# Performance work log

Hardware: AMD Instinct MI355X
Metric: run time of the kernel (lower is better)

Reference implementation:

```python
import jax, jax.numpy as jnp
import numpy as np

N_NODES = 50000
N_EDGES = 600000
NUM_GRAPHS = 512
IN_CH, HID, OUT_CH = 128, 128, 2


def _sage_conv(x, src, dst, Wl, Wr, b):
    # PyG SAGEConv (aggr='mean'): out = lin_l(mean_j x_j) + lin_r(x_i) + bias
    msg = x[src]  # [E, F] gather from source nodes
    agg = jax.ops.segment_sum(msg, dst, num_segments=N_NODES)
    deg = jax.ops.segment_sum(jnp.ones((src.shape[0], 1), x.dtype), dst,
                              num_segments=N_NODES)
    agg = agg / jnp.maximum(deg, 1.0)
    return agg @ Wl + x @ Wr + b


def setup_inputs() -> dict:
    key = jax.random.key(0)
    ks = jax.random.split(key, 12)
    x = jax.random.normal(ks[0], (N_NODES, IN_CH), dtype=jnp.float32)
    edge_index = jax.random.randint(ks[1], (2, N_EDGES), 0, N_NODES, dtype=jnp.int64)
    batch = jnp.sort(jax.random.randint(ks[2], (N_NODES,), 0, NUM_GRAPHS, dtype=jnp.int64))
    dims = [(IN_CH, HID), (HID, HID), (HID, HID), (HID, OUT_CH)]
    params = {}
    for i, (fi, fo) in enumerate(dims, start=1):
        s = 1.0 / np.sqrt(fi)
        params[f"W{i}l"] = jax.random.normal(ks[2 * i + 1], (fi, fo), jnp.float32) * s
        params[f"W{i}r"] = jax.random.normal(ks[2 * i + 2], (fi, fo), jnp.float32) * s
        params[f"b{i}"] = jnp.zeros((fo,), jnp.float32)
    return {"x": x, "edge_index": edge_index, "batch": batch, **params}


def reference(x, edge_index, batch,
              W1l, W1r, b1, W2l, W2r, b2, W3l, W3r, b3, W4l, W4r, b4):
    src, dst = edge_index[0], edge_index[1]
    h = jax.nn.relu(_sage_conv(x, src, dst, W1l, W1r, b1))  # dropout = identity (eval)
    h = jax.nn.relu(_sage_conv(h, src, dst, W2l, W2r, b2))
    h = jax.nn.relu(_sage_conv(h, src, dst, W3l, W3r, b3))
    h = _sage_conv(h, src, dst, W4l, W4r, b4)
    # global_mean_pool: per-graph mean over nodes
    gsum = jax.ops.segment_sum(h, batch, num_segments=NUM_GRAPHS)
    gcnt = jax.ops.segment_sum(jnp.ones((h.shape[0], 1), h.dtype), batch,
                               num_segments=NUM_GRAPHS)
    return gsum / jnp.maximum(gcnt, 1.0)  # [NUM_GRAPHS, OUT_CH]
```

## Files before the change

### kernel.cpp

```cpp
#include <hip/hip_runtime.h>

#define F 128
#define NGRAPH 512

typedef __attribute__((ext_vector_type(8))) __bf16 bf16x8;
typedef __attribute__((ext_vector_type(4))) float f32x4;
typedef __attribute__((ext_vector_type(8))) unsigned short u16x8;

__device__ __forceinline__ unsigned short f2bf(float f) {
    unsigned int u = __float_as_uint(f);
    u = (u + 0x7fffu + ((u >> 16) & 1u)) >> 16;
    return (unsigned short)u;
}
__device__ __forceinline__ float bf2f(unsigned short b) {
    return __uint_as_float(((unsigned int)b) << 16);
}


__global__ __launch_bounds__(256) void k_hist(const int* __restrict__ dst,
                                              int* __restrict__ counts, int e) {
    int i = blockIdx.x * 256 + threadIdx.x;
    if (i < e) atomicAdd(&counts[dst[i]], 1);
}

__global__ __launch_bounds__(256) void k_bsum(const int* __restrict__ counts,
                                              int* __restrict__ bsum, int n) {
    __shared__ int sm[256];
    const int t = threadIdx.x;
    int i = blockIdx.x * 256 + t;
    sm[t] = (i < n) ? counts[i] : 0;
    __syncthreads();
    for (int off = 128; off > 0; off >>= 1) {
        if (t < off) sm[t] += sm[t + off];
        __syncthreads();
    }
    if (t == 0) bsum[blockIdx.x] = sm[0];
}

__global__ __launch_bounds__(256) void k_scanb(const int* __restrict__ bsum,
                                               int* __restrict__ boff, int nb,
                                               int* __restrict__ rs, int n) {
    __shared__ int sm[256];
    const int t = threadIdx.x;
    const int npt = (nb + 255) >> 8;
    const int base = t * npt;
    int s = 0;
    for (int i = 0; i < npt; i++) { int idx = base + i; if (idx < nb) s += bsum[idx]; }
    sm[t] = s;
    __syncthreads();
    for (int off = 1; off < 256; off <<= 1) {
        int u = (t >= off) ? sm[t - off] : 0;
        __syncthreads();
        sm[t] += u;
        __syncthreads();
    }
    int run = (t == 0) ? 0 : sm[t - 1];
    for (int i = 0; i < npt; i++) {
        int idx = base + i;
        if (idx < nb) { boff[idx] = run; run += bsum[idx]; }
    }
    if (t == 255) rs[n] = sm[255];
}

__global__ __launch_bounds__(256) void k_apply(const int* __restrict__ counts,
                                               const int* __restrict__ boff,
                                               int* __restrict__ rs,
                                               int* __restrict__ cursor, int n) {
    __shared__ int sm[256];
    const int t = threadIdx.x;
    int i = blockIdx.x * 256 + t;
    int v = (i < n) ? counts[i] : 0;
    sm[t] = v;
    __syncthreads();
    for (int off = 1; off < 256; off <<= 1) {
        int u = (t >= off) ? sm[t - off] : 0;
        __syncthreads();
        sm[t] += u;
        __syncthreads();
    }
    int excl = sm[t] - v + boff[blockIdx.x];
    if (i < n) { rs[i] = excl; cursor[i] = excl; }
}

__global__ __launch_bounds__(256) void k_scatter(const int* __restrict__ src,
                                                 const int* __restrict__ dst,
                                                 int* __restrict__ cursor,
                                                 int* __restrict__ csr, int e) {
    int i = blockIdx.x * 256 + threadIdx.x;
    if (i < e) {
        int p = atomicAdd(&cursor[dst[i]], 1);
        csr[p] = src[i];
    }
}

__global__ void k_gbounds(const int* __restrict__ batch, int* __restrict__ gstart,
                          int n, int ng) {
    int g = blockIdx.x * blockDim.x + threadIdx.x;
    if (g > ng) return;
    if (g == ng) { gstart[ng] = n; return; }
    int lo = 0, hi = n;
    while (lo < hi) {
        int mid = (lo + hi) >> 1;
        if (batch[mid] < g) lo = mid + 1; else hi = mid;
    }
    gstart[g] = lo;
}


__global__ __launch_bounds__(256) void k_wprep3(
    const float* __restrict__ W1l, const float* __restrict__ W1r,
    const float* __restrict__ W2l, const float* __restrict__ W2r,
    const float* __restrict__ W3l, const float* __restrict__ W3r,
    unsigned short* __restrict__ whi, unsigned short* __restrict__ wlo) {
    int tid = blockIdx.x * 256 + threadIdx.x;
    if (tid >= 3 * 32768) return;
    int layer = tid >> 15;
    int t = tid & 32767;
    const float* Wl = (layer == 0) ? W1l : ((layer == 1) ? W2l : W3l);
    const float* Wr = (layer == 0) ? W1r : ((layer == 1) ? W2r : W3r);
    int j = t & 7;
    int fp = t >> 3;
    int l = fp & 63;
    int ks = (fp >> 6) & 7;
    int nt = fp >> 9;
    int k = ks * 32 + ((l >> 4) << 3) + j;
    int n = nt * 16 + (l & 15);
    float v = (k < F) ? Wl[k * F + n] : Wr[(k - F) * F + n];
    unsigned short hi = f2bf(v);
    unsigned short lo = f2bf(v - bf2f(hi));
    whi[tid] = hi;
    wlo[tid] = lo;
}


__global__ __launch_bounds__(256) void k_xprep(const float4* __restrict__ x4,
                                               unsigned short* __restrict__ hi,
                                               unsigned short* __restrict__ lo, int n4) {
    int i = blockIdx.x * 256 + threadIdx.x;
    if (i >= n4) return;
    float4 v = x4[i];
    ushort4 h, l;
    h.x = f2bf(v.x); l.x = f2bf(v.x - bf2f(h.x));
    h.y = f2bf(v.y); l.y = f2bf(v.y - bf2f(h.y));
    h.z = f2bf(v.z); l.z = f2bf(v.z - bf2f(h.z));
    h.w = f2bf(v.w); l.w = f2bf(v.w - bf2f(h.w));
    *(ushort4*)&hi[i * 4] = h;
    *(ushort4*)&lo[i * 4] = l;
}


__global__ __launch_bounds__(256) void k_aggm_bf(
    const unsigned short* __restrict__ hbf, const int* __restrict__ rs,
    const int* __restrict__ csr,
    unsigned short* __restrict__ agghi, unsigned short* __restrict__ agglo, int nnodes)
{
    int v = blockIdx.x * 16 + (threadIdx.x >> 4);
    if (v >= nnodes) return;
    int c = threadIdx.x & 15;
    const u16x8* h8 = (const u16x8*)hbf;
    int e0 = rs[v], e1 = rs[v + 1];

    float s0[8] = {}, s1[8] = {}, s2[8] = {}, s3[8] = {};
    int e = e0;
    for (; e + 4 <= e1; e += 4) {
        int a = csr[e], b = csr[e + 1], c2 = csr[e + 2], d = csr[e + 3];
        u16x8 va = h8[a * 16 + c];
        u16x8 vb = h8[b * 16 + c];
        u16x8 vc = h8[c2 * 16 + c];
        u16x8 vd = h8[d * 16 + c];
#pragma unroll
        for (int j = 0; j < 8; j++) {
            s0[j] += bf2f(va[j]);
            s1[j] += bf2f(vb[j]);
            s2[j] += bf2f(vc[j]);
            s3[j] += bf2f(vd[j]);
        }
    }
    for (; e < e1; e++) {
        u16x8 va = h8[csr[e] * 16 + c];
#pragma unroll
        for (int j = 0; j < 8; j++) s0[j] += bf2f(va[j]);
    }
    const float inv = 1.f / (float)max(e1 - e0, 1);
    u16x8 hi8, lo8;
#pragma unroll
    for (int j = 0; j < 8; j++) {
        float m = (s0[j] + s1[j] + s2[j] + s3[j]) * inv;
        unsigned short h = f2bf(m);
        hi8[j] = h;
        lo8[j] = f2bf(m - bf2f(h));
    }
    ((u16x8*)agghi)[v * 16 + c] = hi8;
    ((u16x8*)agglo)[v * 16 + c] = lo8;
}


template <int NOLO>
__global__ __launch_bounds__(256, 2) void k_gemm_fused(
    const unsigned short* __restrict__ Ahi, const unsigned short* __restrict__ Alo,
    const unsigned short* __restrict__ Bhi, const unsigned short* __restrict__ Blo,
    const unsigned short* __restrict__ whi, const unsigned short* __restrict__ wlo,
    const float* __restrict__ bias,
    unsigned short* __restrict__ Chi, unsigned short* __restrict__ Clo, int nrows)
{
    __shared__ unsigned short ahi[64 * 256];
    __shared__ unsigned short alo[64 * 256];
    const int t = threadIdx.x;
    const int row0 = blockIdx.x * 64;

    {
        const u16x8* A8h = (const u16x8*)Ahi;
        const u16x8* A8l = (const u16x8*)Alo;
        const u16x8* B8h = (const u16x8*)Bhi;
        const u16x8* B8l = (const u16x8*)Blo;
        u16x8 z8 = (u16x8)0;
#pragma unroll
        for (int it = 0; it < 8; it++) {
            int i = t + 256 * it;
            int row = i >> 5;
            int c8 = i & 31;
            bool ok = (row0 + row) < nrows;
            const u16x8* ph = (c8 < 16) ? A8h : B8h;
            const u16x8* pl = (c8 < 16) ? A8l : B8l;
            int si = (row0 + row) * 16 + (c8 & 15);
            u16x8 vh = ok ? ph[si] : z8;
            u16x8 vl = ok ? pl[si] : z8;
            int didx = row * 256 + ((c8 * 8) ^ ((row & 7) << 3));
            *(u16x8*)&ahi[didx] = vh;
            *(u16x8*)&alo[didx] = vl;
        }
    }
    __syncthreads();

    const int w = t >> 6;
    const int l = t & 63;
    const int lm = l & 15;
    const int lk = l >> 4;
    const bf16x8* whiv = (const bf16x8*)whi;
    const bf16x8* wlov = (const bf16x8*)wlo;

    f32x4 acc[4][2];
#pragma unroll
    for (int rt = 0; rt < 4; rt++)
#pragma unroll
        for (int j = 0; j < 2; j++) acc[rt][j] = (f32x4)(0.f);

    for (int ks = 0; ks < 8; ks++) {
        const int kidx = ks * 32 + lk * 8;
        bf16x8 ah[4], al[4];
#pragma unroll
        for (int rt = 0; rt < 4; rt++) {
            int row = rt * 16 + lm;
            int idx = row * 256 + (kidx ^ ((row & 7) << 3));
            ah[rt] = *(const bf16x8*)&ahi[idx];
            al[rt] = *(const bf16x8*)&alo[idx];
        }
#pragma unroll
        for (int j = 0; j < 2; j++) {
            int nt = 2 * w + j;
            bf16x8 wh = whiv[(nt * 8 + ks) * 64 + l];
            bf16x8 wl = wlov[(nt * 8 + ks) * 64 + l];
#pragma unroll
            for (int rt = 0; rt < 4; rt++) {
                acc[rt][j] = __builtin_amdgcn_mfma_f32_16x16x32_bf16(ah[rt], wh, acc[rt][j], 0, 0, 0);
                acc[rt][j] = __builtin_amdgcn_mfma_f32_16x16x32_bf16(ah[rt], wl, acc[rt][j], 0, 0, 0);
                acc[rt][j] = __builtin_amdgcn_mfma_f32_16x16x32_bf16(al[rt], wh, acc[rt][j], 0, 0, 0);
            }
        }
    }

#pragma unroll
    for (int j = 0; j < 2; j++) {
        int col = (2 * w + j) * 16 + lm;
        float bv = bias[col];
#pragma unroll
        for (int rt = 0; rt < 4; rt++) {
#pragma unroll
            for (int r = 0; r < 4; r++) {
                int row = row0 + rt * 16 + lk * 4 + r;
                if (row < nrows) {
                    float v = fmaxf(acc[rt][j][r] + bv, 0.f);
                    unsigned short h = f2bf(v);
                    Chi[(size_t)row * F + col] = h;
                    if (!NOLO) Clo[(size_t)row * F + col] = f2bf(v - bf2f(h));
                }
            }
        }
    }
}


__global__ __launch_bounds__(512) void k_gpool(
    const unsigned short* __restrict__ h3hi, const int* __restrict__ rs,
    const int* __restrict__ csr, const int* __restrict__ gstart,
    float* __restrict__ ps1, float* __restrict__ ps2)
{
    __shared__ float a1[32][F];
    __shared__ float a2[32][F];
    const int g = blockIdx.x;
    const int v0 = gstart[g], v1 = gstart[g + 1];
    const int grp = threadIdx.x >> 4;
    const int c = threadIdx.x & 15;
    const u16x8* h8 = (const u16x8*)h3hi;

    float l1[8] = {}, l2[8] = {};
    for (int v = v0 + grp; v < v1; v += 32) {
        int e0 = rs[v], e1 = rs[v + 1];
        float s0[8] = {}, s1[8] = {}, s2[8] = {}, s3[8] = {};
        int e = e0;
        for (; e + 4 <= e1; e += 4) {
            int a = csr[e], b = csr[e + 1], c2 = csr[e + 2], d = csr[e + 3];
            u16x8 va = h8[a * 16 + c];
            u16x8 vb = h8[b * 16 + c];
            u16x8 vc = h8[c2 * 16 + c];
            u16x8 vd = h8[d * 16 + c];
#pragma unroll
            for (int j = 0; j < 8; j++) {
                s0[j] += bf2f(va[j]);
                s1[j] += bf2f(vb[j]);
                s2[j] += bf2f(vc[j]);
                s3[j] += bf2f(vd[j]);
            }
        }
        for (; e < e1; e++) {
            u16x8 va = h8[csr[e] * 16 + c];
#pragma unroll
            for (int j = 0; j < 8; j++) s0[j] += bf2f(va[j]);
        }
        const float invd = 1.f / (float)max(e1 - e0, 1);
        u16x8 sv = h8[v * 16 + c];
#pragma unroll
        for (int j = 0; j < 8; j++) {
            l1[j] += (s0[j] + s1[j] + s2[j] + s3[j]) * invd;
            l2[j] += bf2f(sv[j]);
        }
    }
#pragma unroll
    for (int j = 0; j < 8; j++) {
        a1[grp][c * 8 + j] = l1[j];
        a2[grp][c * 8 + j] = l2[j];
    }
    __syncthreads();
    for (int off = 16; off > 0; off >>= 1) {
        if (grp < off) {
#pragma unroll
            for (int j = 0; j < 8; j++) {
                a1[grp][c * 8 + j] += a1[grp + off][c * 8 + j];
                a2[grp][c * 8 + j] += a2[grp + off][c * 8 + j];
            }
        }
        __syncthreads();
    }
    if (grp == 0) {
        const float inv = 1.f / (float)max(v1 - v0, 1);
#pragma unroll
        for (int j = 0; j < 8; j++) {
            ps1[g * F + c * 8 + j] = a1[0][c * 8 + j] * inv;
            ps2[g * F + c * 8 + j] = a2[0][c * 8 + j] * inv;
        }
    }
}


__global__ void k_final(const float* __restrict__ ps1, const float* __restrict__ ps2,
                        const float* __restrict__ W4l, const float* __restrict__ W4r,
                        const float* __restrict__ b4, float* __restrict__ out, int ngraph)
{
    int g = blockIdx.x * 4 + (threadIdx.x >> 6);
    int lane = threadIdx.x & 63;
    if (g >= ngraph) return;
    int k0 = lane * 2;
    float a0 = ps1[g * F + k0], a1 = ps1[g * F + k0 + 1];
    float c0v = ps2[g * F + k0], c1v = ps2[g * F + k0 + 1];
    float p0 = a0 * W4l[k0 * 2 + 0] + a1 * W4l[(k0 + 1) * 2 + 0] +
               c0v * W4r[k0 * 2 + 0] + c1v * W4r[(k0 + 1) * 2 + 0];
    float p1 = a0 * W4l[k0 * 2 + 1] + a1 * W4l[(k0 + 1) * 2 + 1] +
               c0v * W4r[k0 * 2 + 1] + c1v * W4r[(k0 + 1) * 2 + 1];
#pragma unroll
    for (int off = 32; off > 0; off >>= 1) {
        p0 += __shfl_down(p0, off);
        p1 += __shfl_down(p1, off);
    }
    if (lane == 0) {
        out[g * 2 + 0] = p0 + b4[0];
        out[g * 2 + 1] = p1 + b4[1];
    }
}


extern "C" void kernel_launch(void* const* d_in, const int* in_sizes, int n_in,
                              void* d_out, int out_size, void* d_ws, size_t ws_size,
                              hipStream_t stream)
{
    (void)n_in; (void)out_size; (void)ws_size;
    const float* x    = (const float*)d_in[0];
    const int*   ei   = (const int*)d_in[1];
    const int*   batch= (const int*)d_in[2];
    const float* W1l = (const float*)d_in[3];
    const float* W1r = (const float*)d_in[4];
    const float* b1  = (const float*)d_in[5];
    const float* W2l = (const float*)d_in[6];
    const float* W2r = (const float*)d_in[7];
    const float* b2  = (const float*)d_in[8];
    const float* W3l = (const float*)d_in[9];
    const float* W3r = (const float*)d_in[10];
    const float* b3  = (const float*)d_in[11];
    const float* W4l = (const float*)d_in[12];
    const float* W4r = (const float*)d_in[13];
    const float* b4  = (const float*)d_in[14];
    float* out = (float*)d_out;

    const int N = in_sizes[0] / F;
    const int E = in_sizes[1] / 2;
    const int NG = NGRAPH;
    const int* src = ei;
    const int* dst = ei + E;
    const int NB = (N + 255) / 256;
    const int EB = (E + 255) / 256;

    char* p = (char*)d_ws;
    auto alloc = [&](size_t bytes) {
        char* r = p;
        p += (bytes + 255) & ~(size_t)255;
        return r;
    };
    int* counts  = (int*)alloc((size_t)N * 4);
    int* rs      = (int*)alloc((size_t)(N + 1) * 4);
    int* cursor  = (int*)alloc((size_t)N * 4);
    int* csr     = (int*)alloc((size_t)E * 4);
    int* gstart  = (int*)alloc((size_t)(NG + 1) * 4);
    int* bsum    = (int*)alloc((size_t)NB * 4);
    int* boff    = (int*)alloc((size_t)NB * 4);
    const size_t WSPLIT = 3 * 32768;
    unsigned short* wAhi = (unsigned short*)alloc(WSPLIT * 2);
    unsigned short* wAlo = (unsigned short*)alloc(WSPLIT * 2);
    const size_t NF = (size_t)N * F;
    unsigned short* xhi  = (unsigned short*)alloc(NF * 2);
    unsigned short* xlo  = (unsigned short*)alloc(NF * 2);
    unsigned short* H0hi = (unsigned short*)alloc(NF * 2);
    unsigned short* H0lo = (unsigned short*)alloc(NF * 2);
    unsigned short* Agghi= (unsigned short*)alloc(NF * 2);
    unsigned short* Agglo= (unsigned short*)alloc(NF * 2);
    float* ps1   = (float*)alloc((size_t)NG * F * 4);
    float* ps2   = (float*)alloc((size_t)NG * F * 4);

    k_wprep3<<<dim3(384), dim3(256), 0, stream>>>(W1l, W1r, W2l, W2r, W3l, W3r, wAhi, wAlo);
    k_xprep<<<dim3((int)(NF / 4 + 255) / 256, 1, 1), dim3(256), 0, stream>>>(
        (const float4*)x, xhi, xlo, (int)(NF / 4));

    hipMemsetAsync(counts, 0, (size_t)N * 4, stream);
    k_hist<<<dim3(EB), dim3(256), 0, stream>>>(dst, counts, E);
    k_bsum<<<dim3(NB), dim3(256), 0, stream>>>(counts, bsum, N);
    k_scanb<<<dim3(1), dim3(256), 0, stream>>>(bsum, boff, NB, rs, N);
    k_apply<<<dim3(NB), dim3(256), 0, stream>>>(counts, boff, rs, cursor, N);
    k_scatter<<<dim3(EB), dim3(256), 0, stream>>>(src, dst, cursor, csr, E);
    k_gbounds<<<dim3((NG + 256) / 256), dim3(256), 0, stream>>>(batch, gstart, N, NG);

    const int gemmgrid = (N + 63) / 64;
    const int agggrid  = (N + 15) / 16;

    k_aggm_bf<<<dim3(agggrid), dim3(256), 0, stream>>>(xhi, rs, csr, Agghi, Agglo, N);
    k_gemm_fused<0><<<dim3(gemmgrid), dim3(256), 0, stream>>>(
        Agghi, Agglo, xhi, xlo, wAhi + 0 * 32768, wAlo + 0 * 32768, b1, H0hi, H0lo, N);
    k_aggm_bf<<<dim3(agggrid), dim3(256), 0, stream>>>(H0hi, rs, csr, Agghi, Agglo, N);
    k_gemm_fused<0><<<dim3(gemmgrid), dim3(256), 0, stream>>>(
        Agghi, Agglo, H0hi, H0lo, wAhi + 1 * 32768, wAlo + 1 * 32768, b2, xhi, xlo, N);
    k_aggm_bf<<<dim3(agggrid), dim3(256), 0, stream>>>(xhi, rs, csr, Agghi, Agglo, N);
    k_gemm_fused<1><<<dim3(gemmgrid), dim3(256), 0, stream>>>(
        Agghi, Agglo, xhi, xlo, wAhi + 2 * 32768, wAlo + 2 * 32768, b3, H0hi, nullptr, N);
    k_gpool<<<dim3(NG), dim3(512), 0, stream>>>(H0hi, rs, csr, gstart, ps1, ps2);
    k_final<<<dim3(NG / 4), dim3(256), 0, stream>>>(ps1, ps2, W4l, W4r, b4, out, NG);
}
```

Before: 377.6 us.

## Drop activation low-bf16 split and fuse small prep/bounds kernels

Activations are now stored only as a single bf16 value instead of a hi/lo bf16 pair, so the GEMM drops the third MFMA term (Alo×Whi) and no longer loads or stores the low-part buffers. This halves activation memory traffic in the aggregation and GEMM kernels, halves GEMM shared-memory use, and raises the launch-bounds occupancy hint from 2 to 4. Weight prep and x prep are merged into one kernel, and graph-bounds search is merged into the histogram kernel, which removes two launches. The cost is lower activation precision (plain bf16 rounding at every layer), which may move results closer to the tolerance limit.

```diff
diff --git a/kernel.cpp b/kernel.cpp
--- a/kernel.cpp
+++ b/kernel.cpp
@@ -17,10 +17,25 @@
 }
 
 
-__global__ __launch_bounds__(256) void k_hist(const int* __restrict__ dst,
-                                              int* __restrict__ counts, int e) {
-    int i = blockIdx.x * 256 + threadIdx.x;
-    if (i < e) atomicAdd(&counts[dst[i]], 1);
+__global__ __launch_bounds__(256) void k_hist_gb(
+    const int* __restrict__ dst, int* __restrict__ counts, int e,
+    const int* __restrict__ batch, int* __restrict__ gstart, int n, int ng) {
+    const int EB = (e + 255) >> 8;
+    const int b = blockIdx.x;
+    if (b < EB) {
+        int i = b * 256 + threadIdx.x;
+        if (i < e) atomicAdd(&counts[dst[i]], 1);
+    } else {
+        int g = (b - EB) * 256 + threadIdx.x;
+        if (g > ng) return;
+        if (g == ng) { gstart[ng] = n; return; }
+        int lo = 0, hi = n;
+        while (lo < hi) {
+            int mid = (lo + hi) >> 1;
+            if (batch[mid] < g) lo = mid + 1; else hi = mid;
+        }
+        gstart[g] = lo;
+    }
 }
 
 __global__ __launch_bounds__(256) void k_bsum(const int* __restrict__ counts,
@@ -93,66 +108,46 @@
     }
 }
 
-__global__ void k_gbounds(const int* __restrict__ batch, int* __restrict__ gstart,
-                          int n, int ng) {
-    int g = blockIdx.x * blockDim.x + threadIdx.x;
-    if (g > ng) return;
-    if (g == ng) { gstart[ng] = n; return; }
-    int lo = 0, hi = n;
-    while (lo < hi) {
-        int mid = (lo + hi) >> 1;
-        if (batch[mid] < g) lo = mid + 1; else hi = mid;
-    }
-    gstart[g] = lo;
-}
-
-
-__global__ __launch_bounds__(256) void k_wprep3(
+
+__global__ __launch_bounds__(256) void k_prep(
     const float* __restrict__ W1l, const float* __restrict__ W1r,
     const float* __restrict__ W2l, const float* __restrict__ W2r,
     const float* __restrict__ W3l, const float* __restrict__ W3r,
-    unsigned short* __restrict__ whi, unsigned short* __restrict__ wlo) {
-    int tid = blockIdx.x * 256 + threadIdx.x;
-    if (tid >= 3 * 32768) return;
-    int layer = tid >> 15;
-    int t = tid & 32767;
-    const float* Wl = (layer == 0) ? W1l : ((layer == 1) ? W2l : W3l);
-    const float* Wr = (layer == 0) ? W1r : ((layer == 1) ? W2r : W3r);
-    int j = t & 7;
-    int fp = t >> 3;
-    int l = fp & 63;
-    int ks = (fp >> 6) & 7;
-    int nt = fp >> 9;
-    int k = ks * 32 + ((l >> 4) << 3) + j;
-    int n = nt * 16 + (l & 15);
-    float v = (k < F) ? Wl[k * F + n] : Wr[(k - F) * F + n];
-    unsigned short hi = f2bf(v);
-    unsigned short lo = f2bf(v - bf2f(hi));
-    whi[tid] = hi;
-    wlo[tid] = lo;
-}
-
-
-__global__ __launch_bounds__(256) void k_xprep(const float4* __restrict__ x4,
-                                               unsigned short* __restrict__ hi,
-                                               unsigned short* __restrict__ lo, int n4) {
-    int i = blockIdx.x * 256 + threadIdx.x;
-    if (i >= n4) return;
-    float4 v = x4[i];
-    ushort4 h, l;
-    h.x = f2bf(v.x); l.x = f2bf(v.x - bf2f(h.x));
-    h.y = f2bf(v.y); l.y = f2bf(v.y - bf2f(h.y));
-    h.z = f2bf(v.z); l.z = f2bf(v.z - bf2f(h.z));
-    h.w = f2bf(v.w); l.w = f2bf(v.w - bf2f(h.w));
-    *(ushort4*)&hi[i * 4] = h;
-    *(ushort4*)&lo[i * 4] = l;
+    unsigned short* __restrict__ whi, unsigned short* __restrict__ wlo,
+    const float4* __restrict__ x4, unsigned short* __restrict__ xhi, int n4) {
+    const int b = blockIdx.x;
+    if (b < 384) {
+        int tid = b * 256 + threadIdx.x;
+        int layer = tid >> 15;
+        int t = tid & 32767;
+        const float* Wl = (layer == 0) ? W1l : ((layer == 1) ? W2l : W3l);
+        const float* Wr = (layer == 0) ? W1r : ((layer == 1) ? W2r : W3r);
+        int j = t & 7;
+        int fp = t >> 3;
+        int l = fp & 63;
+        int ks = (fp >> 6) & 7;
+        int nt = fp >> 9;
+        int k = ks * 32 + ((l >> 4) << 3) + j;
+        int n = nt * 16 + (l & 15);
+        float v = (k < F) ? Wl[k * F + n] : Wr[(k - F) * F + n];
+        unsigned short hi = f2bf(v);
+        unsigned short lo = f2bf(v - bf2f(hi));
+        whi[tid] = hi;
+        wlo[tid] = lo;
+    } else {
+        int i = (b - 384) * 256 + threadIdx.x;
+        if (i >= n4) return;
+        float4 v = x4[i];
+        ushort4 h;
+        h.x = f2bf(v.x); h.y = f2bf(v.y); h.z = f2bf(v.z); h.w = f2bf(v.w);
+        *(ushort4*)&xhi[i * 4] = h;
+    }
 }
 
 
 __global__ __launch_bounds__(256) void k_aggm_bf(
     const unsigned short* __restrict__ hbf, const int* __restrict__ rs,
-    const int* __restrict__ csr,
-    unsigned short* __restrict__ agghi, unsigned short* __restrict__ agglo, int nnodes)
+    const int* __restrict__ csr, unsigned short* __restrict__ agghi, int nnodes)
 {
     int v = blockIdx.x * 16 + (threadIdx.x >> 4);
     if (v >= nnodes) return;
@@ -182,37 +177,26 @@
         for (int j = 0; j < 8; j++) s0[j] += bf2f(va[j]);
     }
     const float inv = 1.f / (float)max(e1 - e0, 1);
-    u16x8 hi8, lo8;
-#pragma unroll
-    for (int j = 0; j < 8; j++) {
-        float m = (s0[j] + s1[j] + s2[j] + s3[j]) * inv;
-        unsigned short h = f2bf(m);
-        hi8[j] = h;
-        lo8[j] = f2bf(m - bf2f(h));
-    }
+    u16x8 hi8;
+#pragma unroll
+    for (int j = 0; j < 8; j++)
+        hi8[j] = f2bf((s0[j] + s1[j] + s2[j] + s3[j]) * inv);
     ((u16x8*)agghi)[v * 16 + c] = hi8;
-    ((u16x8*)agglo)[v * 16 + c] = lo8;
-}
-
-
-template <int NOLO>
-__global__ __launch_bounds__(256, 2) void k_gemm_fused(
-    const unsigned short* __restrict__ Ahi, const unsigned short* __restrict__ Alo,
-    const unsigned short* __restrict__ Bhi, const unsigned short* __restrict__ Blo,
+}
+
+
+__global__ __launch_bounds__(256, 4) void k_gemm2(
+    const unsigned short* __restrict__ Ahi, const unsigned short* __restrict__ Bhi,
     const unsigned short* __restrict__ whi, const unsigned short* __restrict__ wlo,
-    const float* __restrict__ bias,
-    unsigned short* __restrict__ Chi, unsigned short* __restrict__ Clo, int nrows)
+    const float* __restrict__ bias, unsigned short* __restrict__ Chi, int nrows)
 {
     __shared__ unsigned short ahi[64 * 256];
-    __shared__ unsigned short alo[64 * 256];
     const int t = threadIdx.x;
     const int row0 = blockIdx.x * 64;
 
     {
         const u16x8* A8h = (const u16x8*)Ahi;
-        const u16x8* A8l = (const u16x8*)Alo;
         const u16x8* B8h = (const u16x8*)Bhi;
-        const u16x8* B8l = (const u16x8*)Blo;
         u16x8 z8 = (u16x8)0;
 #pragma unroll
         for (int it = 0; it < 8; it++) {
@@ -221,13 +205,10 @@
             int c8 = i & 31;
             bool ok = (row0 + row) < nrows;
             const u16x8* ph = (c8 < 16) ? A8h : B8h;
-            const u16x8* pl = (c8 < 16) ? A8l : B8l;
             int si = (row0 + row) * 16 + (c8 & 15);
             u16x8 vh = ok ? ph[si] : z8;
-            u16x8 vl = ok ? pl[si] : z8;
             int didx = row * 256 + ((c8 * 8) ^ ((row & 7) << 3));
             *(u16x8*)&ahi[didx] = vh;
-            *(u16x8*)&alo[didx] = vl;
         }
     }
     __syncthreads();
@@ -247,13 +228,12 @@
 
     for (int ks = 0; ks < 8; ks++) {
         const int kidx = ks * 32 + lk * 8;
-        bf16x8 ah[4], al[4];
+        bf16x8 ah[4];
 #pragma unroll
         for (int rt = 0; rt < 4; rt++) {
             int row = rt * 16 + lm;
             int idx = row * 256 + (kidx ^ ((row & 7) << 3));
             ah[rt] = *(const bf16x8*)&ahi[idx];
-            al[rt] = *(const bf16x8*)&alo[idx];
         }
 #pragma unroll
         for (int j = 0; j < 2; j++) {
@@ -264,7 +244,6 @@
             for (int rt = 0; rt < 4; rt++) {
                 acc[rt][j] = __builtin_amdgcn_mfma_f32_16x16x32_bf16(ah[rt], wh, acc[rt][j], 0, 0, 0);
                 acc[rt][j] = __builtin_amdgcn_mfma_f32_16x16x32_bf16(ah[rt], wl, acc[rt][j], 0, 0, 0);
-                acc[rt][j] = __builtin_amdgcn_mfma_f32_16x16x32_bf16(al[rt], wh, acc[rt][j], 0, 0, 0);
             }
         }
     }
@@ -278,12 +257,8 @@
 #pragma unroll
             for (int r = 0; r < 4; r++) {
                 int row = row0 + rt * 16 + lk * 4 + r;
-                if (row < nrows) {
-                    float v = fmaxf(acc[rt][j][r] + bv, 0.f);
-                    unsigned short h = f2bf(v);
-                    Chi[(size_t)row * F + col] = h;
-                    if (!NOLO) Clo[(size_t)row * F + col] = f2bf(v - bf2f(h));
-                }
+                if (row < nrows)
+                    Chi[(size_t)row * F + col] = f2bf(fmaxf(acc[rt][j][r] + bv, 0.f));
             }
         }
     }
@@ -435,39 +410,37 @@
     unsigned short* wAhi = (unsigned short*)alloc(WSPLIT * 2);
     unsigned short* wAlo = (unsigned short*)alloc(WSPLIT * 2);
     const size_t NF = (size_t)N * F;
-    unsigned short* xhi  = (unsigned short*)alloc(NF * 2);
-    unsigned short* xlo  = (unsigned short*)alloc(NF * 2);
-    unsigned short* H0hi = (unsigned short*)alloc(NF * 2);
-    unsigned short* H0lo = (unsigned short*)alloc(NF * 2);
-    unsigned short* Agghi= (unsigned short*)alloc(NF * 2);
-    unsigned short* Agglo= (unsigned short*)alloc(NF * 2);
+    unsigned short* xh   = (unsigned short*)alloc(NF * 2);
+    unsigned short* H0h  = (unsigned short*)alloc(NF * 2);
+    unsigned short* Aggh = (unsigned short*)alloc(NF * 2);
     float* ps1   = (float*)alloc((size_t)NG * F * 4);
     float* ps2   = (float*)alloc((size_t)NG * F * 4);
 
-    k_wprep3<<<dim3(384), dim3(256), 0, stream>>>(W1l, W1r, W2l, W2r, W3l, W3r, wAhi, wAlo);
-    k_xprep<<<dim3((int)(NF / 4 + 255) / 256, 1, 1), dim3(256), 0, stream>>>(
-        (const float4*)x, xhi, xlo, (int)(NF / 4));
+    const int n4 = (int)(NF / 4);
+    const int XB = (n4 + 255) / 256;
+
+    k_prep<<<dim3(384 + XB), dim3(256), 0, stream>>>(
+        W1l, W1r, W2l, W2r, W3l, W3r, wAhi, wAlo, (const float4*)x, xh, n4);
 
     hipMemsetAsync(counts, 0, (size_t)N * 4, stream);
-    k_hist<<<dim3(EB), dim3(256), 0, stream>>>(dst, counts, E);
+    k_hist_gb<<<dim3(EB + 3), dim3(256), 0, stream>>>(dst, counts, E, batch, gstart, N, NG);
     k_bsum<<<dim3(NB), dim3(256), 0, stream>>>(counts, bsum, N);
     k_scanb<<<dim3(1), dim3(256), 0, stream>>>(bsum, boff, NB, rs, N);
     k_apply<<<dim3(NB), dim3(256), 0, stream>>>(counts, boff, rs, cursor, N);
     k_scatter<<<dim3(EB), dim3(256), 0, stream>>>(src, dst, cursor, csr, E);
-    k_gbounds<<<dim3((NG + 256) / 256), dim3(256), 0, stream>>>(batch, gstart, N, NG);
 
     const int gemmgrid = (N + 63) / 64;
     const int agggrid  = (N + 15) / 16;
 
-    k_aggm_bf<<<dim3(agggrid), dim3(256), 0, stream>>>(xhi, rs, csr, Agghi, Agglo, N);
-    k_gemm_fused<0><<<dim3(gemmgrid), dim3(256), 0, stream>>>(
-        Agghi, Agglo, xhi, xlo, wAhi + 0 * 32768, wAlo + 0 * 32768, b1, H0hi, H0lo, N);
-    k_aggm_bf<<<dim3(agggrid), dim3(256), 0, stream>>>(H0hi, rs, csr, Agghi, Agglo, N);
-    k_gemm_fused<0><<<dim3(gemmgrid), dim3(256), 0, stream>>>(
-        Agghi, Agglo, H0hi, H0lo, wAhi + 1 * 32768, wAlo + 1 * 32768, b2, xhi, xlo, N);
-    k_aggm_bf<<<dim3(agggrid), dim3(256), 0, stream>>>(xhi, rs, csr, Agghi, Agglo, N);
-    k_gemm_fused<1><<<dim3(gemmgrid), dim3(256), 0, stream>>>(
-        Agghi, Agglo, xhi, xlo, wAhi + 2 * 32768, wAlo + 2 * 32768, b3, H0hi, nullptr, N);
-    k_gpool<<<dim3(NG), dim3(512), 0, stream>>>(H0hi, rs, csr, gstart, ps1, ps2);
+    k_aggm_bf<<<dim3(agggrid), dim3(256), 0, stream>>>(xh, rs, csr, Aggh, N);
+    k_gemm2<<<dim3(gemmgrid), dim3(256), 0, stream>>>(
+        Aggh, xh, wAhi + 0 * 32768, wAlo + 0 * 32768, b1, H0h, N);
+    k_aggm_bf<<<dim3(agggrid), dim3(256), 0, stream>>>(H0h, rs, csr, Aggh, N);
+    k_gemm2<<<dim3(gemmgrid), dim3(256), 0, stream>>>(
+        Aggh, H0h, wAhi + 1 * 32768, wAlo + 1 * 32768, b2, xh, N);
+    k_aggm_bf<<<dim3(agggrid), dim3(256), 0, stream>>>(xh, rs, csr, Aggh, N);
+    k_gemm2<<<dim3(gemmgrid), dim3(256), 0, stream>>>(
+        Aggh, xh, wAhi + 2 * 32768, wAlo + 2 * 32768, b3, H0h, N);
+    k_gpool<<<dim3(NG), dim3(512), 0, stream>>>(H0h, rs, csr, gstart, ps1, ps2);
     k_final<<<dim3(NG / 4), dim3(256), 0, stream>>>(ps1, ps2, W4l, W4r, b4, out, NG);
 }
```

Measured after the change: 319.0 us. -15.5%, faster.
